# Kernel tuning notes

Hardware: AMD Instinct MI355X
Metric: run time of the kernel (lower is better)

## Reference

```python
import jax, jax.numpy as jnp
import numpy as np

D_MODEL, N_HEADS, D_K = 768, 12, 64
LN_EPS = 1e-5


def setup_inputs() -> dict:
    key = jax.random.key(0)
    ks = jax.random.split(key, 8)
    b, c, n, s = 8, 32, 4, 64
    scale = 1.0 / np.sqrt(D_MODEL)
    inp = {
        "e": jax.random.normal(ks[0], (b, c, n, s, D_MODEL), dtype=jnp.float32),
        "h": jax.random.normal(ks[1], (b, c, s, D_MODEL), dtype=jnp.float32),
        # weights stored [in, out] (torch Linear transposed)
        "Wq": jax.random.normal(ks[2], (D_MODEL, N_HEADS * D_K), dtype=jnp.float32) * scale,
        "bq": jnp.zeros((N_HEADS * D_K,), dtype=jnp.float32),
        "Wk": jax.random.normal(ks[3], (D_MODEL, N_HEADS * D_K), dtype=jnp.float32) * scale,
        "bk": jnp.zeros((N_HEADS * D_K,), dtype=jnp.float32),
        "Wv": jax.random.normal(ks[4], (D_MODEL, N_HEADS * D_K), dtype=jnp.float32) * scale,
        "bv": jnp.zeros((N_HEADS * D_K,), dtype=jnp.float32),
        "Wo": jax.random.normal(ks[5], (N_HEADS * D_K, D_MODEL), dtype=jnp.float32) * scale,
        "bo": jnp.zeros((D_MODEL,), dtype=jnp.float32),
        "ln_g": jnp.ones((D_MODEL,), dtype=jnp.float32),
        "ln_b": jnp.zeros((D_MODEL,), dtype=jnp.float32),
    }
    return inp


def _layer_norm(x, g, b):
    mu = jnp.mean(x, axis=-1, keepdims=True)
    var = jnp.mean(jnp.square(x - mu), axis=-1, keepdims=True)
    return (x - mu) * jax.lax.rsqrt(var + LN_EPS) * g + b


def reference(e, h, Wq, bq, Wk, bk, Wv, bv, Wo, bo, ln_g, ln_b):
    # e: [b, c, n, i, d]  h: [b, c, j, d]
    e_res = e
    en = _layer_norm(e, ln_g, ln_b)
    b, c, n, i, _ = e.shape
    j = h.shape[2]
    q = (en @ Wq + bq).reshape(b, c, n, i, N_HEADS, D_K)
    k = (h @ Wk + bk).reshape(b, c, j, N_HEADS, D_K)
    v = (h @ Wv + bv).reshape(b, c, j, N_HEADS, D_K)
    attn = jnp.einsum('bcnihd,bcjhd->bcnhij', q, k) * (1.0 / np.sqrt(D_K))
    attn = jax.nn.softmax(attn, axis=-1)
    o = jnp.einsum('bcnhij,bcjhd->bcnihd', attn, v).reshape(b, c, n, i, N_HEADS * D_K)
    return o @ Wo + bo + e_res
```

## Files before the change

### kernel.cpp

```cpp
#include <hip/hip_runtime.h>

typedef __bf16 bf16x8 __attribute__((ext_vector_type(8)));
typedef __bf16 bf16x4 __attribute__((ext_vector_type(4)));
typedef float f32x4 __attribute__((ext_vector_type(4)));

__device__ __forceinline__ f32x4 mfma16(bf16x8 a, bf16x8 b, f32x4 c) {
  return __builtin_amdgcn_mfma_f32_16x16x32_bf16(a, b, c, 0, 0, 0);
}

__device__ __forceinline__ void load_lds16(const void* g, void* l) {
  __builtin_amdgcn_global_load_lds(
      (const __attribute__((address_space(1))) void*)g,
      (__attribute__((address_space(3))) void*)l, 16, 0, 0);
}

template <int NWG>
__device__ __forceinline__ int xcd_swz(int orig) {
  constexpr int NX = 8;
  constexpr int q = NWG / NX;
  constexpr int r = NWG % NX;
  const int xcd = orig % NX;
  const int pos = orig / NX;
  if constexpr (r == 0) {
    return xcd * q + pos;
  } else {
    return (xcd < r ? xcd * (q + 1) : r * (q + 1) + (xcd - r) * q) + pos;
  }
}

__global__ __launch_bounds__(256) void prep_w_kernel(
    const float* __restrict__ Wq, const float* __restrict__ Wk,
    const float* __restrict__ Wv, const float* __restrict__ Wo,
    __bf16* __restrict__ WqT, __bf16* __restrict__ WkvT, __bf16* __restrict__ WoT) {
  __shared__ float tile[32][33];
  const int z = blockIdx.z;
  const float* W = (z == 0) ? Wq : (z == 1) ? Wk : (z == 2) ? Wv : Wo;
  __bf16* out = (z == 0) ? WqT : (z == 3) ? WoT : WkvT;
  const int rowOff = (z == 2) ? 768 : 0;
  const int tx = threadIdx.x, ty = threadIdx.y;
  const int x = blockIdx.x * 32 + tx;
  const int y = blockIdx.y * 32 + ty;
#pragma unroll
  for (int i = 0; i < 32; i += 8) tile[ty + i][tx] = W[(size_t)(y + i) * 768 + x];
  __syncthreads();
  const int nx = blockIdx.y * 32 + tx;
  const int ny = blockIdx.x * 32 + ty;
#pragma unroll
  for (int i = 0; i < 32; i += 8)
    out[(size_t)(rowOff + ny + i) * 768 + nx] = (__bf16)tile[tx][ty + i];
}

__global__ __launch_bounds__(256) void ln_kernel(
    const float* __restrict__ e, const float* __restrict__ gam,
    const float* __restrict__ bet, __bf16* __restrict__ en) {
  const int lane = threadIdx.x & 63;
  const int wid = threadIdx.x >> 6;
  const size_t row = (size_t)blockIdx.x * 4 + wid;
  const float* p = e + row * 768;
  float x[12];
  float sum = 0.f;
#pragma unroll
  for (int s = 0; s < 3; ++s) {
    f32x4 v = *(const f32x4*)(p + (s * 64 + lane) * 4);
#pragma unroll
    for (int q = 0; q < 4; ++q) { x[s * 4 + q] = v[q]; sum += v[q]; }
  }
#pragma unroll
  for (int d = 1; d < 64; d <<= 1) sum += __shfl_xor(sum, d);
  const float m = sum * (1.f / 768.f);
  float vs = 0.f;
#pragma unroll
  for (int q = 0; q < 12; ++q) { float d = x[q] - m; vs += d * d; }
#pragma unroll
  for (int d = 1; d < 64; d <<= 1) vs += __shfl_xor(vs, d);
  const float rr = rsqrtf(vs * (1.f / 768.f) + 1e-5f);
  __bf16* o = en + row * 768;
#pragma unroll
  for (int s = 0; s < 3; ++s) {
    f32x4 g4 = *(const f32x4*)(gam + (s * 64 + lane) * 4);
    f32x4 b4 = *(const f32x4*)(bet + (s * 64 + lane) * 4);
    bf16x4 pk;
#pragma unroll
    for (int q = 0; q < 4; ++q) pk[q] = (__bf16)((x[s * 4 + q] - m) * rr * g4[q] + b4[q]);
    *(bf16x4*)(o + (s * 64 + lane) * 4) = pk;
  }
}

__global__ __launch_bounds__(256) void cast_kernel(
    const float* __restrict__ in, __bf16* __restrict__ out, int n4) {
  int i = blockIdx.x * 256 + threadIdx.x;
  const int stride = gridDim.x * 256;
  for (; i < n4; i += stride) {
    f32x4 v = ((const f32x4*)in)[i];
    bf16x4 o;
#pragma unroll
    for (int q = 0; q < 4; ++q) o[q] = (__bf16)v[q];
    ((bf16x4*)out)[i] = o;
  }
}

enum { MODE_Q = 0, MODE_KV = 1, MODE_O = 2 };

template <int MODE, int NC, int NWG>
__global__ __launch_bounds__(512) void gemm_kernel(
    const __bf16* __restrict__ A,
    const __bf16* __restrict__ WT,
    const float* __restrict__ bias0, const float* __restrict__ bias1,
    const float* __restrict__ eres,
    __bf16* __restrict__ dst0, __bf16* __restrict__ dst1,
    float* __restrict__ outp) {
  __shared__ __bf16 As[2][16384];
  __shared__ __bf16 Bs[2][16384];
  const int wgid = xcd_swz<NWG>(blockIdx.x);
  const int rowBase = (wgid / NC) * 256;
  const int colBase = (wgid % NC) * 256;
  const int t = threadIdx.x;
  const int lane = t & 63, wid = t >> 6;
  const int wm = wid >> 2, wn = wid & 3;
  const int lr = lane & 15, lg = lane >> 4;
  const int srow = t >> 3;
  const int skcol = ((t & 7) ^ (srow & 7)) * 8;
  f32x4 acc[8][4] = {};

  auto stage = [&](int kbb, int buf) {
#pragma unroll
    for (int p = 0; p < 4; ++p) {
      const int rowIn = p * 64 + srow;
      const __bf16* ga;
      if constexpr (MODE == MODE_O) {
        const int r = rowBase + rowIn;
        ga = A + ((((size_t)(r >> 6)) * 12 + kbb) << 12) + ((r & 63) << 6) + skcol;
      } else {
        ga = A + (size_t)(rowBase + rowIn) * 768 + kbb * 64 + skcol;
      }
      load_lds16(ga, &As[buf][p * 4096 + t * 8]);
      const __bf16* gb = WT + (size_t)(colBase + rowIn) * 768 + kbb * 64 + skcol;
      load_lds16(gb, &Bs[buf][p * 4096 + t * 8]);
    }
  };
  auto compute = [&](int buf) {
#pragma unroll
    for (int kc = 0; kc < 2; ++kc) {
      const int c8 = (kc * 4 + lg) ^ (lr & 7);
      bf16x8 a[8], b[4];
#pragma unroll
      for (int it = 0; it < 8; ++it)
        a[it] = *(const bf16x8*)&As[buf][(wm * 128 + it * 16 + lr) * 64 + c8 * 8];
#pragma unroll
      for (int jt = 0; jt < 4; ++jt)
        b[jt] = *(const bf16x8*)&Bs[buf][(wn * 64 + jt * 16 + lr) * 64 + c8 * 8];
#pragma unroll
      for (int it = 0; it < 8; ++it)
#pragma unroll
        for (int jt = 0; jt < 4; ++jt)
          acc[it][jt] = mfma16(a[it], b[jt], acc[it][jt]);
    }
  };

  stage(0, 0);
  stage(1, 1);
#pragma unroll
  for (int kb = 0; kb < 12; ++kb) {
    if (kb < 11) {
      asm volatile("s_waitcnt vmcnt(8)" ::: "memory");
    } else {
      asm volatile("s_waitcnt vmcnt(0)" ::: "memory");
    }
    __builtin_amdgcn_sched_barrier(0);
    __builtin_amdgcn_s_barrier();
    compute(kb & 1);
    __builtin_amdgcn_s_barrier();
    if (kb < 10) stage(kb + 2, kb & 1);
  }

  const int roww = rowBase + wm * 128;
  const int colw = colBase + wn * 64;
#pragma unroll
  for (int it = 0; it < 8; ++it) {
#pragma unroll
    for (int jt = 0; jt < 4; ++jt) {
      const int c = colw + jt * 16 + lr;
#pragma unroll
      for (int rg = 0; rg < 4; ++rg) {
        const int r = roww + it * 16 + lg * 4 + rg;
        const float val = acc[it][jt][rg];
        if constexpr (MODE == MODE_O) {
          outp[(size_t)r * 768 + c] = val + bias0[c] + eres[(size_t)r * 768 + c];
        } else if constexpr (MODE == MODE_Q) {
          dst0[((((size_t)(r >> 6)) * 12 + (c >> 6)) << 12) + ((r & 63) << 6) + (c & 63)] =
              (__bf16)(val + bias0[c]);
        } else {
          if (c < 768) {
            dst0[((((size_t)(r >> 6)) * 12 + (c >> 6)) << 12) + ((r & 63) << 6) + (c & 63)] =
                (__bf16)(val + bias0[c]);
          } else {
            const int c2 = c - 768;
            dst1[((((size_t)(r >> 6)) * 12 + (c2 >> 6)) << 12) + ((c2 & 63) << 6) + (r & 63)] =
                (__bf16)(val + bias1[c2]);
          }
        }
      }
    }
  }
}

__global__ __launch_bounds__(256) void attn_kernel(
    const __bf16* __restrict__ q, const __bf16* __restrict__ k,
    const __bf16* __restrict__ v, __bf16* __restrict__ o) {
  const int bh = blockIdx.x;
  const int h = bh % 12;
  const int bc = bh / 12;
  const int t = threadIdx.x;
  const int wid = t >> 6, lane = t & 63;
  const int lr = lane & 15, lg = lane >> 4;
  __shared__ __bf16 kL[64][72];
  __shared__ __bf16 vL[64][72];
  __shared__ __bf16 P[4][64][72];

  {
    const __bf16* kp = k + ((size_t)bh << 12);
    const __bf16* vp = v + ((size_t)bh << 12);
    const int row = t >> 2, col = (t & 3) * 16;
    *(bf16x8*)&kL[row][col]     = *(const bf16x8*)(kp + row * 64 + col);
    *(bf16x8*)&kL[row][col + 8] = *(const bf16x8*)(kp + row * 64 + col + 8);
    *(bf16x8*)&vL[row][col]     = *(const bf16x8*)(vp + row * 64 + col);
    *(bf16x8*)&vL[row][col + 8] = *(const bf16x8*)(vp + row * 64 + col + 8);
  }
  const __bf16* qp = q + (((size_t)(bc * 4 + wid) * 12 + h) << 12);
  __bf16* op = o + (((size_t)(bc * 4 + wid) * 12 + h) << 12);
  bf16x8 qf[4][2];
#pragma unroll
  for (int it = 0; it < 4; ++it)
#pragma unroll
    for (int kc = 0; kc < 2; ++kc)
      qf[it][kc] = *(const bf16x8*)(qp + (it * 16 + lr) * 64 + kc * 32 + lg * 8);
  __syncthreads();

  f32x4 s[4][4] = {};
#pragma unroll
  for (int kc = 0; kc < 2; ++kc) {
    bf16x8 kf[4];
#pragma unroll
    for (int jt = 0; jt < 4; ++jt)
      kf[jt] = *(const bf16x8*)&kL[jt * 16 + lr][kc * 32 + lg * 8];
#pragma unroll
    for (int jt = 0; jt < 4; ++jt)
#pragma unroll
      for (int it = 0; it < 4; ++it)
        s[jt][it] = mfma16(kf[jt], qf[it][kc], s[jt][it]);
  }

  float recip[4];
#pragma unroll
  for (int it = 0; it < 4; ++it) {
    float m = -1e30f;
#pragma unroll
    for (int jt = 0; jt < 4; ++jt)
#pragma unroll
      for (int rg = 0; rg < 4; ++rg) m = fmaxf(m, s[jt][it][rg]);
    m = fmaxf(m, __shfl_xor(m, 16));
    m = fmaxf(m, __shfl_xor(m, 32));
    float sum = 0.f;
#pragma unroll
    for (int jt = 0; jt < 4; ++jt) {
      bf16x4 pk;
#pragma unroll
      for (int rg = 0; rg < 4; ++rg) {
        float p = __expf((s[jt][it][rg] - m) * 0.125f);
        sum += p;
        pk[rg] = (__bf16)p;
      }
      *(bf16x4*)&P[wid][it * 16 + lr][jt * 16 + lg * 4] = pk;
    }
    sum += __shfl_xor(sum, 16);
    sum += __shfl_xor(sum, 32);
    recip[it] = 1.f / sum;
  }

  f32x4 oacc[4][4] = {};
#pragma unroll
  for (int kc = 0; kc < 2; ++kc) {
    bf16x8 vf[4], pf[4];
#pragma unroll
    for (int dt = 0; dt < 4; ++dt)
      vf[dt] = *(const bf16x8*)&vL[dt * 16 + lr][kc * 32 + lg * 8];
#pragma unroll
    for (int it = 0; it < 4; ++it)
      pf[it] = *(const bf16x8*)&P[wid][it * 16 + lr][kc * 32 + lg * 8];
#pragma unroll
    for (int dt = 0; dt < 4; ++dt)
#pragma unroll
      for (int it = 0; it < 4; ++it)
        oacc[dt][it] = mfma16(vf[dt], pf[it], oacc[dt][it]);
  }
#pragma unroll
  for (int it = 0; it < 4; ++it) {
    const float rc = recip[it];
#pragma unroll
    for (int dt = 0; dt < 4; ++dt) {
      bf16x4 pk;
#pragma unroll
      for (int rg = 0; rg < 4; ++rg) pk[rg] = (__bf16)(oacc[dt][it][rg] * rc);
      *(bf16x4*)(op + (size_t)(it * 16 + lr) * 64 + dt * 16 + lg * 4) = pk;
    }
  }
}

extern "C" void kernel_launch(void* const* d_in, const int* in_sizes, int n_in,
                              void* d_out, int out_size, void* d_ws, size_t ws_size,
                              hipStream_t stream) {
  const float* e  = (const float*)d_in[0];
  const float* h  = (const float*)d_in[1];
  const float* Wq = (const float*)d_in[2];
  const float* bq = (const float*)d_in[3];
  const float* Wk = (const float*)d_in[4];
  const float* bk = (const float*)d_in[5];
  const float* Wv = (const float*)d_in[6];
  const float* bv = (const float*)d_in[7];
  const float* Wo = (const float*)d_in[8];
  const float* bo = (const float*)d_in[9];
  const float* g  = (const float*)d_in[10];
  const float* b  = (const float*)d_in[11];
  float* outp = (float*)d_out;
  char* ws = (char*)d_ws;

  __bf16* WqT  = (__bf16*)(ws);
  __bf16* WkvT = (__bf16*)(ws + 1179648);
  __bf16* WoT  = (__bf16*)(ws + 3538944);
  char* R1 = ws + 4718592;
  __bf16* en    = (__bf16*)(R1);
  __bf16* h_bf  = (__bf16*)(R1);
  __bf16* k_ws  = (__bf16*)(R1 + 25165824);
  __bf16* v_ws  = (__bf16*)(R1 + 50331648);
  __bf16* q_ws  = (__bf16*)(ws + 105381888);

  prep_w_kernel<<<dim3(24, 24, 4), dim3(32, 8), 0, stream>>>(Wq, Wk, Wv, Wo, WqT, WkvT, WoT);
  ln_kernel<<<16384, 256, 0, stream>>>(e, g, b, en);
  gemm_kernel<MODE_Q, 3, 768><<<768, 512, 0, stream>>>(
      en, WqT, bq, nullptr, nullptr, q_ws, nullptr, nullptr);
  cast_kernel<<<2048, 256, 0, stream>>>(h, h_bf, 16384 * 768 / 4);
  gemm_kernel<MODE_KV, 6, 384><<<384, 512, 0, stream>>>(
      h_bf, WkvT, bk, bv, nullptr, k_ws, v_ws, nullptr);
  attn_kernel<<<3072, 256, 0, stream>>>(q_ws, k_ws, v_ws, q_ws);
  gemm_kernel<MODE_O, 3, 768><<<768, 512, 0, stream>>>(
      q_ws, WoT, bo, nullptr, e, nullptr, nullptr, outp);
}
```

Measured before the change: 494.5 us.

## Shrink GEMM tile to 128x256 with triple-buffered LDS and interleaved loads

The GEMM kernel now uses 128-row tiles instead of 256, doubling the workgroup count, and moves from two LDS buffers to three. Global-to-LDS loads for stage k+2 are split into halves placed between the two MFMA phases, and each MFMA phase is wrapped in s_setprio. The goal is better CU occupancy and load balance across the grid, plus closer overlap of memory and matrix work. The cost is lower per-tile data reuse, since the weight tiles are reloaded twice as often.

After: 491.5 us. Within noise of the previous version (-0.6%).

```diff
diff --git a/kernel.cpp b/kernel.cpp
--- a/kernel.cpp
+++ b/kernel.cpp
@@ -109,10 +109,10 @@
     const float* __restrict__ eres,
     __bf16* __restrict__ dst0, __bf16* __restrict__ dst1,
     float* __restrict__ outp) {
-  __shared__ __bf16 As[2][16384];
-  __shared__ __bf16 Bs[2][16384];
+  __shared__ __bf16 As[3][8192];
+  __shared__ __bf16 Bs[3][16384];
   const int wgid = xcd_swz<NWG>(blockIdx.x);
-  const int rowBase = (wgid / NC) * 256;
+  const int rowBase = (wgid / NC) * 128;
   const int colBase = (wgid % NC) * 256;
   const int t = threadIdx.x;
   const int lane = t & 63, wid = t >> 6;
@@ -120,63 +120,73 @@
   const int lr = lane & 15, lg = lane >> 4;
   const int srow = t >> 3;
   const int skcol = ((t & 7) ^ (srow & 7)) * 8;
-  f32x4 acc[8][4] = {};
-
-  auto stage = [&](int kbb, int buf) {
-#pragma unroll
-    for (int p = 0; p < 4; ++p) {
-      const int rowIn = p * 64 + srow;
-      const __bf16* ga;
-      if constexpr (MODE == MODE_O) {
-        const int r = rowBase + rowIn;
-        ga = A + ((((size_t)(r >> 6)) * 12 + kbb) << 12) + ((r & 63) << 6) + skcol;
-      } else {
-        ga = A + (size_t)(rowBase + rowIn) * 768 + kbb * 64 + skcol;
-      }
-      load_lds16(ga, &As[buf][p * 4096 + t * 8]);
-      const __bf16* gb = WT + (size_t)(colBase + rowIn) * 768 + kbb * 64 + skcol;
-      load_lds16(gb, &Bs[buf][p * 4096 + t * 8]);
-    }
+  f32x4 acc[4][4] = {};
+
+  auto stageA = [&](int kbb, int p, int buf) {
+    const int rowIn = p * 64 + srow;
+    const __bf16* ga;
+    if constexpr (MODE == MODE_O) {
+      const int r = rowBase + rowIn;
+      ga = A + ((((size_t)(r >> 6)) * 12 + kbb) << 12) + ((r & 63) << 6) + skcol;
+    } else {
+      ga = A + (size_t)(rowBase + rowIn) * 768 + kbb * 64 + skcol;
+    }
+    load_lds16(ga, &As[buf][p * 4096 + t * 8]);
   };
-  auto compute = [&](int buf) {
-#pragma unroll
-    for (int kc = 0; kc < 2; ++kc) {
-      const int c8 = (kc * 4 + lg) ^ (lr & 7);
-      bf16x8 a[8], b[4];
-#pragma unroll
-      for (int it = 0; it < 8; ++it)
-        a[it] = *(const bf16x8*)&As[buf][(wm * 128 + it * 16 + lr) * 64 + c8 * 8];
+  auto stageB = [&](int kbb, int p, int buf) {
+    const int rowIn = p * 64 + srow;
+    const __bf16* gb = WT + (size_t)(colBase + rowIn) * 768 + kbb * 64 + skcol;
+    load_lds16(gb, &Bs[buf][p * 4096 + t * 8]);
+  };
+  auto phase = [&](int buf, int kc) {
+    const int c8 = (kc * 4 + lg) ^ (lr & 7);
+    bf16x8 a[4], b[4];
+#pragma unroll
+    for (int it = 0; it < 4; ++it)
+      a[it] = *(const bf16x8*)&As[buf][(wm * 64 + it * 16 + lr) * 64 + c8 * 8];
+#pragma unroll
+    for (int jt = 0; jt < 4; ++jt)
+      b[jt] = *(const bf16x8*)&Bs[buf][(wn * 64 + jt * 16 + lr) * 64 + c8 * 8];
+    asm volatile("s_waitcnt lgkmcnt(0)" ::: "memory");
+    __builtin_amdgcn_sched_barrier(0);
+    __builtin_amdgcn_s_setprio(1);
+#pragma unroll
+    for (int it = 0; it < 4; ++it)
 #pragma unroll
       for (int jt = 0; jt < 4; ++jt)
-        b[jt] = *(const bf16x8*)&Bs[buf][(wn * 64 + jt * 16 + lr) * 64 + c8 * 8];
-#pragma unroll
-      for (int it = 0; it < 8; ++it)
-#pragma unroll
-        for (int jt = 0; jt < 4; ++jt)
-          acc[it][jt] = mfma16(a[it], b[jt], acc[it][jt]);
-    }
+        acc[it][jt] = mfma16(a[it], b[jt], acc[it][jt]);
+    __builtin_amdgcn_s_setprio(0);
+    __builtin_amdgcn_sched_barrier(0);
   };
 
-  stage(0, 0);
-  stage(1, 1);
+  {
+    stageA(0, 0, 0); stageA(0, 1, 0);
+    stageB(0, 0, 0); stageB(0, 1, 0); stageB(0, 2, 0); stageB(0, 3, 0);
+    stageA(1, 0, 1); stageA(1, 1, 1);
+    stageB(1, 0, 1); stageB(1, 1, 1); stageB(1, 2, 1); stageB(1, 3, 1);
+  }
 #pragma unroll
   for (int kb = 0; kb < 12; ++kb) {
-    if (kb < 11) {
-      asm volatile("s_waitcnt vmcnt(8)" ::: "memory");
+    const int buf = kb % 3;
+    const int nbuf = (kb + 2) % 3;
+    if (kb <= 10) {
+      asm volatile("s_waitcnt vmcnt(6)" ::: "memory");
     } else {
       asm volatile("s_waitcnt vmcnt(0)" ::: "memory");
     }
     __builtin_amdgcn_sched_barrier(0);
     __builtin_amdgcn_s_barrier();
-    compute(kb & 1);
+    if (kb <= 9) { stageA(kb + 2, 0, nbuf); stageB(kb + 2, 0, nbuf); stageB(kb + 2, 1, nbuf); }
+    phase(buf, 0);
+    if (kb <= 9) { stageA(kb + 2, 1, nbuf); stageB(kb + 2, 2, nbuf); stageB(kb + 2, 3, nbuf); }
+    phase(buf, 1);
     __builtin_amdgcn_s_barrier();
-    if (kb < 10) stage(kb + 2, kb & 1);
-  }
-
-  const int roww = rowBase + wm * 128;
+  }
+
+  const int roww = rowBase + wm * 64;
   const int colw = colBase + wn * 64;
 #pragma unroll
-  for (int it = 0; it < 8; ++it) {
+  for (int it = 0; it < 4; ++it) {
 #pragma unroll
     for (int jt = 0; jt < 4; ++jt) {
       const int c = colw + jt * 16 + lr;
@@ -336,12 +346,12 @@
 
   prep_w_kernel<<<dim3(24, 24, 4), dim3(32, 8), 0, stream>>>(Wq, Wk, Wv, Wo, WqT, WkvT, WoT);
   ln_kernel<<<16384, 256, 0, stream>>>(e, g, b, en);
-  gemm_kernel<MODE_Q, 3, 768><<<768, 512, 0, stream>>>(
+  gemm_kernel<MODE_Q, 3, 1536><<<1536, 512, 0, stream>>>(
       en, WqT, bq, nullptr, nullptr, q_ws, nullptr, nullptr);
   cast_kernel<<<2048, 256, 0, stream>>>(h, h_bf, 16384 * 768 / 4);
-  gemm_kernel<MODE_KV, 6, 384><<<384, 512, 0, stream>>>(
+  gemm_kernel<MODE_KV, 6, 768><<<768, 512, 0, stream>>>(
       h_bf, WkvT, bk, bv, nullptr, k_ws, v_ws, nullptr);
   attn_kernel<<<3072, 256, 0, stream>>>(q_ws, k_ws, v_ws, q_ws);
-  gemm_kernel<MODE_O, 3, 768><<<768, 512, 0, stream>>>(
+  gemm_kernel<MODE_O, 3, 1536><<<1536, 512, 0, stream>>>(
       q_ws, WoT, bo, nullptr, e, nullptr, nullptr, outp);
 }
```

## Use persistent 128x128-tile GEMM with cross-tile pipelined loads

Applied to the files above, without the earlier changes.

Shrinks the GEMM tile from 256x256 with 512 threads to 128x128 with 256 threads. Each of 512 persistent workgroups now walks several tiles in sequence, and the double-buffered K pipeline carries over tile boundaries so the next tile's loads are issued during the current tile's epilogue. The goal is a balanced grid of 512 workgroups on 256 CUs instead of 768 or 384 large-tile workgroups, which leave a ragged tail wave. The trade-off is lower data reuse per tile and more global/LDS traffic per FLOP.

New measurement: 534.5 us. +8.1%, slower.

```diff
diff --git a/kernel.cpp b/kernel.cpp
--- a/kernel.cpp
+++ b/kernel.cpp
@@ -101,31 +101,35 @@
 
 enum { MODE_Q = 0, MODE_KV = 1, MODE_O = 2 };
 
-template <int MODE, int NC, int NWG>
-__global__ __launch_bounds__(512) void gemm_kernel(
+template <int MODE, int NR, int TPB>
+__global__ __launch_bounds__(256) void gemm_kernel(
     const __bf16* __restrict__ A,
     const __bf16* __restrict__ WT,
     const float* __restrict__ bias0, const float* __restrict__ bias1,
     const float* __restrict__ eres,
     __bf16* __restrict__ dst0, __bf16* __restrict__ dst1,
     float* __restrict__ outp) {
-  __shared__ __bf16 As[2][16384];
-  __shared__ __bf16 Bs[2][16384];
-  const int wgid = xcd_swz<NWG>(blockIdx.x);
-  const int rowBase = (wgid / NC) * 256;
-  const int colBase = (wgid % NC) * 256;
+  __shared__ __bf16 As[2][8192];
+  __shared__ __bf16 Bs[2][8192];
+  const int tile0 = xcd_swz<512>(blockIdx.x) * TPB;
   const int t = threadIdx.x;
   const int lane = t & 63, wid = t >> 6;
-  const int wm = wid >> 2, wn = wid & 3;
+  const int wm = wid >> 1, wn = wid & 1;
   const int lr = lane & 15, lg = lane >> 4;
-  const int srow = t >> 3;
-  const int skcol = ((t & 7) ^ (srow & 7)) * 8;
-  f32x4 acc[8][4] = {};
-
-  auto stage = [&](int kbb, int buf) {
-#pragma unroll
-    for (int p = 0; p < 4; ++p) {
-      const int rowIn = p * 64 + srow;
+  const int srow = lane >> 3;
+  const int skcol = ((lane & 7) ^ srow) * 8;
+  f32x4 acc[4][4] = {};
+  constexpr int G = TPB * 12;
+
+  auto stage = [&](int g, int buf) {
+    const int tl = tile0 + g / 12;
+    const int kbb = g % 12;
+    const int rowBase = (tl % NR) * 128;
+    const int colBase = (tl / NR) * 128;
+#pragma unroll
+    for (int s = 0; s < 4; ++s) {
+      const int chunk = s * 4 + wid;
+      const int rowIn = chunk * 8 + srow;
       const __bf16* ga;
       if constexpr (MODE == MODE_O) {
         const int r = rowBase + rowIn;
@@ -133,74 +137,78 @@
       } else {
         ga = A + (size_t)(rowBase + rowIn) * 768 + kbb * 64 + skcol;
       }
-      load_lds16(ga, &As[buf][p * 4096 + t * 8]);
+      load_lds16(ga, &As[buf][chunk * 512]);
       const __bf16* gb = WT + (size_t)(colBase + rowIn) * 768 + kbb * 64 + skcol;
-      load_lds16(gb, &Bs[buf][p * 4096 + t * 8]);
+      load_lds16(gb, &Bs[buf][chunk * 512]);
     }
   };
   auto compute = [&](int buf) {
 #pragma unroll
     for (int kc = 0; kc < 2; ++kc) {
+      bf16x8 a[4], b[4];
       const int c8 = (kc * 4 + lg) ^ (lr & 7);
-      bf16x8 a[8], b[4];
-#pragma unroll
-      for (int it = 0; it < 8; ++it)
-        a[it] = *(const bf16x8*)&As[buf][(wm * 128 + it * 16 + lr) * 64 + c8 * 8];
+#pragma unroll
+      for (int it = 0; it < 4; ++it)
+        a[it] = *(const bf16x8*)&As[buf][(wm * 64 + it * 16 + lr) * 64 + c8 * 8];
 #pragma unroll
       for (int jt = 0; jt < 4; ++jt)
         b[jt] = *(const bf16x8*)&Bs[buf][(wn * 64 + jt * 16 + lr) * 64 + c8 * 8];
 #pragma unroll
-      for (int it = 0; it < 8; ++it)
+      for (int it = 0; it < 4; ++it)
 #pragma unroll
         for (int jt = 0; jt < 4; ++jt)
           acc[it][jt] = mfma16(a[it], b[jt], acc[it][jt]);
     }
   };
-
-  stage(0, 0);
-  stage(1, 1);
-#pragma unroll
-  for (int kb = 0; kb < 12; ++kb) {
-    if (kb < 11) {
-      asm volatile("s_waitcnt vmcnt(8)" ::: "memory");
-    } else {
-      asm volatile("s_waitcnt vmcnt(0)" ::: "memory");
-    }
-    __builtin_amdgcn_sched_barrier(0);
-    __builtin_amdgcn_s_barrier();
-    compute(kb & 1);
-    __builtin_amdgcn_s_barrier();
-    if (kb < 10) stage(kb + 2, kb & 1);
-  }
-
-  const int roww = rowBase + wm * 128;
-  const int colw = colBase + wn * 64;
-#pragma unroll
-  for (int it = 0; it < 8; ++it) {
-#pragma unroll
-    for (int jt = 0; jt < 4; ++jt) {
-      const int c = colw + jt * 16 + lr;
-#pragma unroll
-      for (int rg = 0; rg < 4; ++rg) {
-        const int r = roww + it * 16 + lg * 4 + rg;
-        const float val = acc[it][jt][rg];
-        if constexpr (MODE == MODE_O) {
-          outp[(size_t)r * 768 + c] = val + bias0[c] + eres[(size_t)r * 768 + c];
-        } else if constexpr (MODE == MODE_Q) {
-          dst0[((((size_t)(r >> 6)) * 12 + (c >> 6)) << 12) + ((r & 63) << 6) + (c & 63)] =
-              (__bf16)(val + bias0[c]);
-        } else {
-          if (c < 768) {
+  auto epilogue = [&](int tl) {
+    const int rowBase = (tl % NR) * 128;
+    const int colBase = (tl / NR) * 128;
+    const int roww = rowBase + wm * 64;
+    const int colw = colBase + wn * 64;
+#pragma unroll
+    for (int it = 0; it < 4; ++it) {
+#pragma unroll
+      for (int jt = 0; jt < 4; ++jt) {
+        const int c = colw + jt * 16 + lr;
+#pragma unroll
+        for (int rg = 0; rg < 4; ++rg) {
+          const int r = roww + it * 16 + lg * 4 + rg;
+          const float val = acc[it][jt][rg];
+          if constexpr (MODE == MODE_O) {
+            outp[(size_t)r * 768 + c] = val + bias0[c] + eres[(size_t)r * 768 + c];
+          } else if constexpr (MODE == MODE_Q) {
             dst0[((((size_t)(r >> 6)) * 12 + (c >> 6)) << 12) + ((r & 63) << 6) + (c & 63)] =
                 (__bf16)(val + bias0[c]);
           } else {
-            const int c2 = c - 768;
-            dst1[((((size_t)(r >> 6)) * 12 + (c2 >> 6)) << 12) + ((c2 & 63) << 6) + (r & 63)] =
-                (__bf16)(val + bias1[c2]);
+            if (c < 768) {
+              dst0[((((size_t)(r >> 6)) * 12 + (c >> 6)) << 12) + ((r & 63) << 6) + (c & 63)] =
+                  (__bf16)(val + bias0[c]);
+            } else {
+              const int c2 = c - 768;
+              dst1[((((size_t)(r >> 6)) * 12 + (c2 >> 6)) << 12) + ((c2 & 63) << 6) + (r & 63)] =
+                  (__bf16)(val + bias1[c2]);
+            }
           }
+          acc[it][jt][rg] = 0.f;
         }
       }
     }
+  };
+
+  stage(0, 0);
+  stage(1, 1);
+  for (int g = 0; g < G; ++g) {
+    if (g == G - 1) {
+      asm volatile("s_waitcnt vmcnt(0)" ::: "memory");
+    } else {
+      asm volatile("s_waitcnt vmcnt(8)" ::: "memory");
+    }
+    __builtin_amdgcn_sched_barrier(0);
+    __builtin_amdgcn_s_barrier();
+    compute(g & 1);
+    __builtin_amdgcn_s_barrier();
+    if ((g % 12) == 11) epilogue(tile0 + g / 12);
+    if (g + 2 < G) stage(g + 2, g & 1);
   }
 }
 
@@ -336,12 +344,12 @@
 
   prep_w_kernel<<<dim3(24, 24, 4), dim3(32, 8), 0, stream>>>(Wq, Wk, Wv, Wo, WqT, WkvT, WoT);
   ln_kernel<<<16384, 256, 0, stream>>>(e, g, b, en);
-  gemm_kernel<MODE_Q, 3, 768><<<768, 512, 0, stream>>>(
+  gemm_kernel<MODE_Q, 512, 6><<<512, 256, 0, stream>>>(
       en, WqT, bq, nullptr, nullptr, q_ws, nullptr, nullptr);
   cast_kernel<<<2048, 256, 0, stream>>>(h, h_bf, 16384 * 768 / 4);
-  gemm_kernel<MODE_KV, 6, 384><<<384, 512, 0, stream>>>(
+  gemm_kernel<MODE_KV, 128, 3><<<512, 256, 0, stream>>>(
       h_bf, WkvT, bk, bv, nullptr, k_ws, v_ws, nullptr);
   attn_kernel<<<3072, 256, 0, stream>>>(q_ws, k_ws, v_ws, q_ws);
-  gemm_kernel<MODE_O, 3, 768><<<768, 512, 0, stream>>>(
+  gemm_kernel<MODE_O, 512, 6><<<512, 256, 0, stream>>>(
       q_ws, WoT, bo, nullptr, e, nullptr, nullptr, outp);
 }
```

## Restructure GEMM mainloop into 4-stage K=32 pipeline with split A/B staging

Applied to the files above, without the earlier changes.

The GEMM mainloop drops K=64 double buffering for a 4-slot ring of K=32 tiles, issuing stages three tiles ahead. Each iteration runs in two halves. The A and B global-to-LDS loads for future tiles are interleaved between the halves, and s_setprio raises priority around the MFMA blocks. The aim is to hide global load latency better and overlap LDS reads with MFMA work. The cost is twice as many barriers per unit of K and more complex vmcnt accounting, while LDS footprint stays the same.

Result: faster. 481.6 us (-2.6%).

```diff
diff --git a/kernel.cpp b/kernel.cpp
--- a/kernel.cpp
+++ b/kernel.cpp
@@ -102,15 +102,15 @@
 enum { MODE_Q = 0, MODE_KV = 1, MODE_O = 2 };
 
 template <int MODE, int NC, int NWG>
-__global__ __launch_bounds__(512) void gemm_kernel(
+__global__ __launch_bounds__(512) void gemm8_kernel(
     const __bf16* __restrict__ A,
     const __bf16* __restrict__ WT,
     const float* __restrict__ bias0, const float* __restrict__ bias1,
     const float* __restrict__ eres,
     __bf16* __restrict__ dst0, __bf16* __restrict__ dst1,
     float* __restrict__ outp) {
-  __shared__ __bf16 As[2][16384];
-  __shared__ __bf16 Bs[2][16384];
+  __shared__ __bf16 As[4 * 8192];
+  __shared__ __bf16 Bs[4 * 8192];
   const int wgid = xcd_swz<NWG>(blockIdx.x);
   const int rowBase = (wgid / NC) * 256;
   const int colBase = (wgid % NC) * 256;
@@ -118,59 +118,87 @@
   const int lane = t & 63, wid = t >> 6;
   const int wm = wid >> 2, wn = wid & 3;
   const int lr = lane & 15, lg = lane >> 4;
-  const int srow = t >> 3;
-  const int skcol = ((t & 7) ^ (srow & 7)) * 8;
+  const int srow = t >> 2;
+  const int skcol = ((t & 3) ^ (srow & 3)) * 8;
+  const int cg = lg ^ (lr & 3);
   f32x4 acc[8][4] = {};
 
-  auto stage = [&](int kbb, int buf) {
-#pragma unroll
-    for (int p = 0; p < 4; ++p) {
-      const int rowIn = p * 64 + srow;
+  auto stageA = [&](int kt) {
+    const int slot = kt & 3;
+#pragma unroll
+    for (int p = 0; p < 2; ++p) {
+      const int rowIn = p * 128 + srow;
       const __bf16* ga;
       if constexpr (MODE == MODE_O) {
         const int r = rowBase + rowIn;
-        ga = A + ((((size_t)(r >> 6)) * 12 + kbb) << 12) + ((r & 63) << 6) + skcol;
+        ga = A + ((((size_t)(r >> 6)) * 12 + (kt >> 1)) << 12) + ((r & 63) << 6) +
+             (kt & 1) * 32 + skcol;
       } else {
-        ga = A + (size_t)(rowBase + rowIn) * 768 + kbb * 64 + skcol;
+        ga = A + (size_t)(rowBase + rowIn) * 768 + kt * 32 + skcol;
       }
-      load_lds16(ga, &As[buf][p * 4096 + t * 8]);
-      const __bf16* gb = WT + (size_t)(colBase + rowIn) * 768 + kbb * 64 + skcol;
-      load_lds16(gb, &Bs[buf][p * 4096 + t * 8]);
+      load_lds16(ga, &As[slot * 8192 + p * 4096 + t * 8]);
     }
   };
-  auto compute = [&](int buf) {
-#pragma unroll
-    for (int kc = 0; kc < 2; ++kc) {
-      const int c8 = (kc * 4 + lg) ^ (lr & 7);
-      bf16x8 a[8], b[4];
-#pragma unroll
-      for (int it = 0; it < 8; ++it)
-        a[it] = *(const bf16x8*)&As[buf][(wm * 128 + it * 16 + lr) * 64 + c8 * 8];
-#pragma unroll
-      for (int jt = 0; jt < 4; ++jt)
-        b[jt] = *(const bf16x8*)&Bs[buf][(wn * 64 + jt * 16 + lr) * 64 + c8 * 8];
-#pragma unroll
-      for (int it = 0; it < 8; ++it)
-#pragma unroll
-        for (int jt = 0; jt < 4; ++jt)
-          acc[it][jt] = mfma16(a[it], b[jt], acc[it][jt]);
+  auto stageB = [&](int kt) {
+    const int slot = kt & 3;
+#pragma unroll
+    for (int p = 0; p < 2; ++p) {
+      const int rowIn = p * 128 + srow;
+      const __bf16* gb = WT + (size_t)(colBase + rowIn) * 768 + kt * 32 + skcol;
+      load_lds16(gb, &Bs[slot * 8192 + p * 4096 + t * 8]);
     }
   };
 
-  stage(0, 0);
-  stage(1, 1);
-#pragma unroll
-  for (int kb = 0; kb < 12; ++kb) {
-    if (kb < 11) {
+  stageA(0); stageB(0);
+  stageA(1); stageB(1);
+  stageA(2); stageB(2);
+
+#pragma unroll
+  for (int kt = 0; kt < 24; ++kt) {
+    const int slot = kt & 3;
+    if (kt <= 21) {
       asm volatile("s_waitcnt vmcnt(8)" ::: "memory");
+    } else if (kt == 22) {
+      asm volatile("s_waitcnt vmcnt(4)" ::: "memory");
     } else {
       asm volatile("s_waitcnt vmcnt(0)" ::: "memory");
     }
     __builtin_amdgcn_sched_barrier(0);
     __builtin_amdgcn_s_barrier();
-    compute(kb & 1);
+
+    bf16x8 b[4], a0[4];
+#pragma unroll
+    for (int it = 0; it < 4; ++it)
+      a0[it] = *(const bf16x8*)&As[slot * 8192 + (wm * 128 + it * 16 + lr) * 32 + cg * 8];
+#pragma unroll
+    for (int jt = 0; jt < 4; ++jt)
+      b[jt] = *(const bf16x8*)&Bs[slot * 8192 + (wn * 64 + jt * 16 + lr) * 32 + cg * 8];
+    if (kt + 3 < 24) stageA(kt + 3);
+    asm volatile("s_waitcnt lgkmcnt(0)" ::: "memory");
+    __builtin_amdgcn_sched_barrier(0);
+    __builtin_amdgcn_s_setprio(1);
+#pragma unroll
+    for (int it = 0; it < 4; ++it)
+#pragma unroll
+      for (int jt = 0; jt < 4; ++jt)
+        acc[it][jt] = mfma16(a0[it], b[jt], acc[it][jt]);
+    __builtin_amdgcn_s_setprio(0);
     __builtin_amdgcn_s_barrier();
-    if (kb < 10) stage(kb + 2, kb & 1);
+
+    bf16x8 a1[4];
+#pragma unroll
+    for (int it = 0; it < 4; ++it)
+      a1[it] = *(const bf16x8*)&As[slot * 8192 + (wm * 128 + (it + 4) * 16 + lr) * 32 + cg * 8];
+    if (kt + 3 < 24) stageB(kt + 3);
+    asm volatile("s_waitcnt lgkmcnt(0)" ::: "memory");
+    __builtin_amdgcn_sched_barrier(0);
+    __builtin_amdgcn_s_setprio(1);
+#pragma unroll
+    for (int it = 0; it < 4; ++it)
+#pragma unroll
+      for (int jt = 0; jt < 4; ++jt)
+        acc[it + 4][jt] = mfma16(a1[it], b[jt], acc[it + 4][jt]);
+    __builtin_amdgcn_s_setprio(0);
   }
 
   const int roww = rowBase + wm * 128;
@@ -336,12 +364,12 @@
 
   prep_w_kernel<<<dim3(24, 24, 4), dim3(32, 8), 0, stream>>>(Wq, Wk, Wv, Wo, WqT, WkvT, WoT);
   ln_kernel<<<16384, 256, 0, stream>>>(e, g, b, en);
-  gemm_kernel<MODE_Q, 3, 768><<<768, 512, 0, stream>>>(
+  gemm8_kernel<MODE_Q, 3, 768><<<768, 512, 0, stream>>>(
       en, WqT, bq, nullptr, nullptr, q_ws, nullptr, nullptr);
   cast_kernel<<<2048, 256, 0, stream>>>(h, h_bf, 16384 * 768 / 4);
-  gemm_kernel<MODE_KV, 6, 384><<<384, 512, 0, stream>>>(
+  gemm8_kernel<MODE_KV, 6, 384><<<384, 512, 0, stream>>>(
       h_bf, WkvT, bk, bv, nullptr, k_ws, v_ws, nullptr);
   attn_kernel<<<3072, 256, 0, stream>>>(q_ws, k_ws, v_ws, q_ws);
-  gemm_kernel<MODE_O, 3, 768><<<768, 512, 0, stream>>>(
+  gemm8_kernel<MODE_O, 3, 768><<<768, 512, 0, stream>>>(
       q_ws, WoT, bo, nullptr, e, nullptr, nullptr, outp);
 }
```
